# Optimization experiments

Measured on AMD Instinct MI355X. Metric: run time of the kernel, lower is better.

The kernel has to match this reference:

```python
import jax, jax.numpy as jnp
import numpy as np

N_NODES = 8192
N_EDGES = 131072

_DIMS = [
    ("cnn1", 3, 32), ("cnn2", 32, 64), ("cnn3", 64, 128),
    ("gcn1", 128, 256), ("gcn2", 256, 512), ("gcn3", 512, 1024),
    ("cnnd1", 1024, 512), ("cnnd2", 512, 256), ("cnnd3", 256, 128), ("cnnd4", 128, 50),
]


def setup_inputs() -> dict:
    key = jax.random.key(0)
    ks = jax.random.split(key, 2 + 2 * len(_DIMS))
    inp = {
        "x": jax.random.normal(ks[0], (N_NODES, 3), dtype=jnp.float32),
        "edge_index": jax.random.randint(ks[1], (2, N_EDGES), 0, N_NODES, dtype=jnp.int64)
        if jax.config.jax_enable_x64 else
        jax.random.randint(ks[1], (2, N_EDGES), 0, N_NODES, dtype=jnp.int32),
    }
    for i, (name, din, dout) in enumerate(_DIMS):
        scale = 1.0 / np.sqrt(din)
        inp[name + "_w"] = jax.random.normal(ks[2 + 2 * i], (din, dout), dtype=jnp.float32) * scale
        inp[name + "_b"] = jax.random.normal(ks[3 + 2 * i], (dout,), dtype=jnp.float32) * scale
    return inp


def _gcn_norm(edge_index, n, dtype):
    # add self-loops, symmetric normalization D^{-1/2}(A+I)D^{-1/2}
    loop = jnp.arange(n, dtype=edge_index.dtype)
    src = jnp.concatenate([edge_index[0], loop])
    dst = jnp.concatenate([edge_index[1], loop])
    deg = jax.ops.segment_sum(jnp.ones_like(dst, dtype=dtype), dst, num_segments=n)
    dinv = jnp.where(deg > 0, 1.0 / jnp.sqrt(deg), 0.0)
    norm = dinv[src] * dinv[dst]  # [E+N]
    return src, dst, norm


def _forward(x, edge_index,
             cnn1_w, cnn1_b, cnn2_w, cnn2_b, cnn3_w, cnn3_b,
             gcn1_w, gcn1_b, gcn2_w, gcn2_b, gcn3_w, gcn3_b,
             cnnd1_w, cnnd1_b, cnnd2_w, cnnd2_b, cnnd3_w, cnnd3_b, cnnd4_w, cnnd4_b):
    n = x.shape[0]
    src, dst, norm = _gcn_norm(edge_index, n, x.dtype)

    def lin(h, w, b):  # 1x1 Conv1d == per-node linear
        return h @ w + b

    def gcn(h, w, b):
        hl = h @ w                                    # [N, out]
        msg = hl[src] * norm[:, None]                 # gather + scale [E+N, out]
        return jax.ops.segment_sum(msg, dst, num_segments=n) + b

    h = jax.nn.relu(lin(x, cnn1_w, cnn1_b))
    h = jax.nn.relu(lin(h, cnn2_w, cnn2_b))
    h = jax.nn.relu(lin(h, cnn3_w, cnn3_b))
    h = jax.nn.relu(gcn(h, gcn1_w, gcn1_b))
    h = jax.nn.relu(gcn(h, gcn2_w, gcn2_b))
    h = jax.nn.relu(gcn(h, gcn3_w, gcn3_b))
    h = jax.nn.relu(lin(h, cnnd1_w, cnnd1_b))
    h = jax.nn.relu(lin(h, cnnd2_w, cnnd2_b))
    h = jax.nn.relu(lin(h, cnnd3_w, cnnd3_b))
    h = lin(h, cnnd4_w, cnnd4_b)
    return jax.nn.softmax(h, axis=1)  # [N, output_dim]


def reference(x, edge_index,
              cnn1_w, cnn1_b, cnn2_w, cnn2_b, cnn3_w, cnn3_b,
              gcn1_w, gcn1_b, gcn2_w, gcn2_b, gcn3_w, gcn3_b,
              cnnd1_w, cnnd1_b, cnnd2_w, cnnd2_b, cnnd3_w, cnnd3_b, cnnd4_w, cnnd4_b):
    return _forward(x, edge_index,
                    cnn1_w, cnn1_b, cnn2_w, cnn2_b, cnn3_w, cnn3_b,
                    gcn1_w, gcn1_b, gcn2_w, gcn2_b, gcn3_w, gcn3_b,
                    cnnd1_w, cnnd1_b, cnnd2_w, cnnd2_b, cnnd3_w, cnnd3_b, cnnd4_w, cnnd4_b)
```

## Files before the change

kernel.cpp:

```cpp
#include <hip/hip_runtime.h>
#include <math.h>

#define N_NODES 8192
#define N_EDGES 131072

typedef unsigned short u16;
typedef unsigned int u32;
typedef short bf16x8 __attribute__((ext_vector_type(8)));
typedef int v4i __attribute__((ext_vector_type(4)));
typedef float f32x4 __attribute__((ext_vector_type(4)));

__device__ __forceinline__ u16 f2bf(float x) {
    unsigned u = __float_as_uint(x);
    u += 0x7fffu + ((u >> 16) & 1u);
    return (u16)(u >> 16);
}
__device__ __forceinline__ float bf2f(u16 h) { return __uint_as_float(((unsigned)h) << 16); }

#define GLD_LDS(gp, lp) __builtin_amdgcn_global_load_lds( \
    (const __attribute__((address_space(1))) void*)(gp),  \
    (__attribute__((address_space(3))) void*)(lp), 16, 0, 0)

template <int N> __device__ __forceinline__ void wait_vmcnt() {
    if constexpr (N == 0) asm volatile("s_waitcnt vmcnt(0)" ::: "memory");
    else if constexpr (N == 4) asm volatile("s_waitcnt vmcnt(4)" ::: "memory");
    else static_assert(N < 0, "unsupported vmcnt");
}

__device__ __forceinline__ u32 lds_addr(const void* p) {
    return (u32)(size_t)(const __attribute__((address_space(3))) void*)p;
}

__device__ __forceinline__ bf16x8 lds_read_b128(u32 addr) {
    v4i r;
    asm volatile("ds_read_b128 %0, %1" : "=v"(r) : "v"(addr));
    union { v4i i; bf16x8 b; } u;
    u.i = r;
    return u.b;
}

template <int NU> struct UV;
template <> struct UV<1> { typedef u32 T; };
template <> struct UV<2> { typedef uint2 T; };
template <> struct UV<4> { typedef uint4 T; };


__global__ void k_count(const int* __restrict__ ei, int* __restrict__ deg) {
    int e = blockIdx.x * 256 + threadIdx.x;
    if (e < N_EDGES) atomicAdd(&deg[ei[N_EDGES + e]], 1);
}

__global__ __launch_bounds__(1024) void k_scan(const int* __restrict__ deg,
                                               int* __restrict__ rowptr,
                                               int* __restrict__ pos,
                                               float* __restrict__ dinv) {
    __shared__ int sums[1024];
    int t = threadIdx.x;
    int local[8];
    int s = 0;
#pragma unroll
    for (int i = 0; i < 8; ++i) {
        local[i] = deg[t * 8 + i];
        dinv[t * 8 + i] = 1.0f / sqrtf((float)(local[i] + 1));
        s += local[i];
    }
    sums[t] = s;
    __syncthreads();
    for (int off = 1; off < 1024; off <<= 1) {
        int v = (t >= off) ? sums[t - off] : 0;
        __syncthreads();
        sums[t] += v;
        __syncthreads();
    }
    int run = sums[t] - s;
#pragma unroll
    for (int i = 0; i < 8; ++i) {
        rowptr[t * 8 + i] = run;
        pos[t * 8 + i] = run;
        run += local[i];
    }
    if (t == 1023) rowptr[8192] = run;
}

__global__ void k_fill(const int* __restrict__ ei, const float* __restrict__ dinv,
                       int* __restrict__ pos, int* __restrict__ csr_src,
                       float* __restrict__ csr_w) {
    int e = blockIdx.x * 256 + threadIdx.x;
    if (e < N_EDGES) {
        int s = ei[e];
        int t = ei[N_EDGES + e];
        int idx = atomicAdd(&pos[t], 1);
        csr_src[idx] = s;
        csr_w[idx] = dinv[s] * dinv[t];
    }
}

__global__ void k_prep_all(const float* __restrict__ g1w, const float* __restrict__ g2w,
                           const float* __restrict__ g3w, const float* __restrict__ d1w,
                           const float* __restrict__ d2w, const float* __restrict__ d3w,
                           u16* __restrict__ wts, int* __restrict__ deg) {
    int idx = blockIdx.x * 256 + threadIdx.x;
    if (idx < N_NODES) deg[idx] = 0;
    const float* W;
    int local, lgK, N;
    u16 *hi, *lo;
    if (idx < 32768)        { W = g1w; local = idx;           lgK = 7;  N = 256;  hi = wts;           lo = wts + 32768; }
    else if (idx < 163840)  { W = g2w; local = idx - 32768;   lgK = 8;  N = 512;  hi = wts + 65536;   lo = wts + 196608; }
    else if (idx < 688128)  { W = g3w; local = idx - 163840;  lgK = 9;  N = 1024; hi = wts + 327680;  lo = wts + 851968; }
    else if (idx < 1212416) { W = d1w; local = idx - 688128;  lgK = 10; N = 512;  hi = wts + 1376256; lo = wts + 1900544; }
    else if (idx < 1343488) { W = d2w; local = idx - 1212416; lgK = 9;  N = 256;  hi = wts + 2424832; lo = wts + 2555904; }
    else if (idx < 1376256) { W = d3w; local = idx - 1343488; lgK = 8;  N = 128;  hi = wts + 2686976; lo = wts + 2719744; }
    else return;
    int n = local >> lgK;
    int k = local & ((1 << lgK) - 1);
    float v = W[(size_t)k * N + n];
    u16 h = f2bf(v);
    int dst = ((k >> 3) * N + n) * 8 + (k & 7);
    hi[dst] = h;
    lo[dst] = f2bf(v - bf2f(h));
}

__global__ __launch_bounds__(256) void k_enc_fused(const float* __restrict__ x,
                                                   const float* __restrict__ w1, const float* __restrict__ b1,
                                                   const float* __restrict__ w2, const float* __restrict__ b2,
                                                   const float* __restrict__ w3, const float* __restrict__ b3,
                                                   u16* __restrict__ Chi, u16* __restrict__ Clo) {
    __shared__ float lw[10560];
    const int tid = threadIdx.x;
    for (int i = tid; i < 96; i += 256) lw[i] = w1[i];
    for (int i = tid; i < 32; i += 256) lw[96 + i] = b1[i];
    for (int i = tid; i < 2048; i += 256) lw[128 + i] = w2[i];
    for (int i = tid; i < 64; i += 256) lw[2176 + i] = b2[i];
    for (int i = tid; i < 8192; i += 256) lw[2240 + i] = w3[i];
    for (int i = tid; i < 128; i += 256) lw[10432 + i] = b3[i];
    __syncthreads();

    const int lane = tid & 63;
    const int node = blockIdx.x * 4 + (tid >> 6);

    float x0 = x[node * 3 + 0], x1 = x[node * 3 + 1], x2 = x[node * 3 + 2];

    int o1 = lane & 31;
    float h1 = fmaxf(x0 * lw[o1] + x1 * lw[32 + o1] + x2 * lw[64 + o1] + lw[96 + o1], 0.f);

    float h2 = lw[2176 + lane];
#pragma unroll
    for (int k = 0; k < 32; ++k) h2 += __shfl(h1, k) * lw[128 + k * 64 + lane];
    h2 = fmaxf(h2, 0.f);

    float h3a = lw[10432 + lane];
    float h3b = lw[10432 + 64 + lane];
#pragma unroll
    for (int k = 0; k < 64; ++k) {
        float hk = __shfl(h2, k);
        h3a += hk * lw[2240 + k * 128 + lane];
        h3b += hk * lw[2240 + k * 128 + 64 + lane];
    }
    h3a = fmaxf(h3a, 0.f);
    h3b = fmaxf(h3b, 0.f);

    size_t base = (size_t)node * 128;
    u16 ha = f2bf(h3a), hb = f2bf(h3b);
    Chi[base + lane] = ha;
    Chi[base + 64 + lane] = hb;
    Clo[base + lane] = f2bf(h3a - bf2f(ha));
    Clo[base + 64 + lane] = f2bf(h3b - bf2f(hb));
}

__global__ __launch_bounds__(256) void k_d4sm_fused(const float* __restrict__ A,
                                                    const float* __restrict__ W,
                                                    const float* __restrict__ bias,
                                                    float* __restrict__ out) {
    __shared__ float lw[6450];
    const int tid = threadIdx.x;
    for (int i = tid; i < 6400; i += 256) lw[i] = W[i];
    for (int i = tid; i < 50; i += 256) lw[6400 + i] = bias[i];
    __syncthreads();

    const int lane = tid & 63;
    const int node = blockIdx.x * 4 + (tid >> 6);

    float a0 = A[(size_t)node * 128 + lane];
    float a1 = A[(size_t)node * 128 + 64 + lane];

    float acc = (lane < 50) ? lw[6400 + lane] : 0.f;
    int oc = (lane < 50) ? lane : 0;
#pragma unroll
    for (int k = 0; k < 64; ++k) acc += __shfl(a0, k) * lw[k * 50 + oc];
#pragma unroll
    for (int k = 0; k < 64; ++k) acc += __shfl(a1, k) * lw[(64 + k) * 50 + oc];

    float v = (lane < 50) ? acc : -INFINITY;
    float m = v;
#pragma unroll
    for (int off = 32; off; off >>= 1) m = fmaxf(m, __shfl_xor(m, off));
    float e = (lane < 50) ? expf(v - m) : 0.f;
    float s = e;
#pragma unroll
    for (int off = 32; off; off >>= 1) s += __shfl_xor(s, off);
    if (lane < 50) out[(size_t)node * 50 + lane] = e / s;
}

template <int D>
__global__ __launch_bounds__(256) void k_agg_s(const u16* __restrict__ hi_in,
                                               const u16* __restrict__ lo_in,
                                               u16* __restrict__ hi_out,
                                               u16* __restrict__ lo_out,
                                               const int* __restrict__ rowptr,
                                               const int* __restrict__ csr_src,
                                               const float* __restrict__ csr_w,
                                               const float* __restrict__ dinv) {
    constexpr int EPL = D / 64;
    constexpr int NU = EPL / 2;
    using VT = typename UV<NU>::T;
    int node = blockIdx.x * 4 + (threadIdx.x >> 6);
    int lane = threadIdx.x & 63;
    const size_t off = (size_t)node * D + lane * EPL;
    float acc[EPL];
    {
        float dn = dinv[node];
        float w0 = dn * dn;
        u32 hu[NU], lu[NU];
        *(VT*)hu = *(const VT*)(hi_in + off);
        *(VT*)lu = *(const VT*)(lo_in + off);
#pragma unroll
        for (int j = 0; j < NU; ++j) {
            acc[2 * j]     = (__uint_as_float(hu[j] << 16) + __uint_as_float(lu[j] << 16)) * w0;
            acc[2 * j + 1] = (__uint_as_float(hu[j] & 0xffff0000u) + __uint_as_float(lu[j] & 0xffff0000u)) * w0;
        }
    }
#define EDGE_ACC(S, W) do {                                                            \
        size_t so = (size_t)(S) * D + lane * EPL;                                      \
        u32 hu[NU], lu[NU];                                                            \
        *(VT*)hu = *(const VT*)(hi_in + so);                                           \
        *(VT*)lu = *(const VT*)(lo_in + so);                                           \
        _Pragma("unroll")                                                              \
        for (int j = 0; j < NU; ++j) {                                                 \
            acc[2 * j]     += (__uint_as_float(hu[j] << 16) + __uint_as_float(lu[j] << 16)) * (W); \
            acc[2 * j + 1] += (__uint_as_float(hu[j] & 0xffff0000u) + __uint_as_float(lu[j] & 0xffff0000u)) * (W); \
        }                                                                              \
    } while (0)
    int beg = rowptr[node], end = rowptr[node + 1];
    int e = beg;
    for (; e + 2 <= end; e += 2) {
        int s0 = csr_src[e], s1 = csr_src[e + 1];
        float wa = csr_w[e], wb = csr_w[e + 1];
        EDGE_ACC(s0, wa);
        EDGE_ACC(s1, wb);
    }
    if (e < end) EDGE_ACC(csr_src[e], csr_w[e]);
#undef EDGE_ACC
    u32 how[NU], low[NU];
#pragma unroll
    for (int j = 0; j < NU; ++j) {
        u16 h0 = f2bf(acc[2 * j]);     u16 l0 = f2bf(acc[2 * j] - bf2f(h0));
        u16 h1 = f2bf(acc[2 * j + 1]); u16 l1 = f2bf(acc[2 * j + 1] - bf2f(h1));
        how[j] = (u32)h0 | ((u32)h1 << 16);
        low[j] = (u32)l0 | ((u32)l1 << 16);
    }
    *(VT*)(hi_out + off) = *(VT*)how;
    *(VT*)(lo_out + off) = *(VT*)low;
}

template <int D>
__global__ __launch_bounds__(256) void k_agg(const float* __restrict__ h, float* __restrict__ out,
                                             const int* __restrict__ rowptr,
                                             const int* __restrict__ csr_src,
                                             const float* __restrict__ csr_w,
                                             const float* __restrict__ dinv) {
    constexpr int NF2 = D / 128;
    int node = blockIdx.x * 4 + (threadIdx.x >> 6);
    int lane = threadIdx.x & 63;
    const float2* hn = (const float2*)(h + (size_t)node * D);
    float dn = dinv[node];
    float w0 = dn * dn;
    float2 acc[NF2];
#pragma unroll
    for (int j = 0; j < NF2; ++j) {
        float2 v = hn[lane + j * 64];
        acc[j].x = v.x * w0;
        acc[j].y = v.y * w0;
    }
    int beg = rowptr[node], end = rowptr[node + 1];
    for (int e = beg; e < end; ++e) {
        int s = csr_src[e];
        float w = csr_w[e];
        const float2* hs = (const float2*)(h + (size_t)s * D);
#pragma unroll
        for (int j = 0; j < NF2; ++j) {
            float2 v = hs[lane + j * 64];
            acc[j].x += v.x * w;
            acc[j].y += v.y * w;
        }
    }
    float2* op = (float2*)(out + (size_t)node * D);
#pragma unroll
    for (int j = 0; j < NF2; ++j) op[lane + j * 64] = acc[j];
}

template <int OUTS>
__global__ __launch_bounds__(64) void k_linear_small(const float* __restrict__ A,
                                                     const float* __restrict__ W,
                                                     const float* __restrict__ bias,
                                                     float* __restrict__ Cf,
                                                     u16* __restrict__ Chi,
                                                     u16* __restrict__ Clo,
                                                     int K, int N, int relu) {
    int n = blockIdx.y;
    int o = blockIdx.x * 64 + threadIdx.x;
    if (o >= N) return;
    float s = bias[o];
    const float* a = A + (size_t)n * K;
    for (int k = 0; k < K; ++k) s += a[k] * W[(size_t)k * N + o];
    if (relu) s = fmaxf(s, 0.0f);
    if (OUTS == 0) {
        Cf[(size_t)n * N + o] = s;
    } else {
        u16 h = f2bf(s);
        Chi[(size_t)n * N + o] = h;
        Clo[(size_t)n * N + o] = f2bf(s - bf2f(h));
    }
}

template <int OUTS>
__global__ __launch_bounds__(256, 2) void k_gemm_mfma(
    const u16* __restrict__ Ahi, const u16* __restrict__ Alo,
    const u16* __restrict__ Bhi, const u16* __restrict__ Blo,
    const float* __restrict__ bias,
    float* __restrict__ Cf, u16* __restrict__ Chi, u16* __restrict__ Clo,
    int M, int N, int K, int relu) {
    constexpr int BM = 128, BN = 128, WN = 32;
    constexpr int BK = 32;
    constexpr int FM = BM / 16, FN = WN / 16;
    constexpr int ASZ = (BK / 8) * BM * 16;
    constexpr int TOT = 2 * ASZ;
    constexpr int NSTG = TOT / 4096;

    __shared__ char lds0[TOT] __attribute__((aligned(16)));
    __shared__ char lds1[TOT] __attribute__((aligned(16)));

    const int tid = threadIdx.x;
    const int lane = tid & 63;
    const int wave = tid >> 6;

    const int nwg = gridDim.x * gridDim.y;
    const int d = blockIdx.y * gridDim.x + blockIdx.x;
    const int q = nwg >> 3;
    const int lg = (d & 7) * q + (d >> 3);
    const int bx = lg % gridDim.x, by = lg / gridDim.x;
    const int m0 = by * BM, n0 = bx * BN;

    const u16* gp[NSTG];
    int ldo[NSTG];
#pragma unroll
    for (int i = 0; i < NSTG; ++i) {
        int o = i * 4096 + tid * 16;
        ldo[i] = o;
        const u16* base;
        int roff;
        if (o < ASZ) { base = Ahi; roff = o; }
        else         { base = Alo; roff = o - ASZ; }
        int c = roff / (BM * 16);
        int r = (roff % (BM * 16)) / 16;
        gp[i] = base + (size_t)(m0 + r) * K + c * 8;
    }

    const int kc = lane >> 4, rr = lane & 15;
    const int aoff = (kc * BM + rr) * 16;

    const size_t bbase = ((size_t)kc * N + n0 + wave * WN + rr) * 8;
    const size_t bstep = (size_t)4 * N * 8;

    f32x4 acc[FM][FN];
#pragma unroll
    for (int i = 0; i < FM; ++i)
#pragma unroll
        for (int j = 0; j < FN; ++j) acc[i][j] = f32x4{0.f, 0.f, 0.f, 0.f};

    bf16x8 b0h[FN], b0l[FN], b1h[FN], b1l[FN];

#define STAGE(P, KS) do {                                          \
        _Pragma("unroll")                                          \
        for (int i = 0; i < NSTG; ++i)                             \
            GLD_LDS(gp[i] + (KS) * BK, (P) + ldo[i]);              \
    } while (0)

#define LOADB(BH, BL, KS) do {                                                      \
        _Pragma("unroll")                                                           \
        for (int fn = 0; fn < FN; ++fn) {                                           \
            BH[fn] = *(const bf16x8*)(Bhi + bbase + (size_t)(KS) * bstep + fn * 128); \
            BL[fn] = *(const bf16x8*)(Blo + bbase + (size_t)(KS) * bstep + fn * 128); \
        }                                                                           \
    } while (0)

#define STEP(CUR, DST, BHC, BLC, BHD, BLD, KS) do {                                 \
        if ((KS) + 1 < nks) LOADB(BHD, BLD, (KS) + 1);                              \
        __builtin_amdgcn_sched_barrier(0);                                          \
        if ((KS) + 1 < nks) wait_vmcnt<4>(); else wait_vmcnt<0>();                  \
        asm volatile("s_barrier" ::: "memory");                                     \
        if ((KS) + 1 < nks) STAGE(DST, (KS) + 1);                                   \
        const u32 pb_ = lds_addr(CUR);                                              \
        bf16x8 ah[FM], al[FM];                                                      \
        _Pragma("unroll")                                                           \
        for (int fm = 0; fm < FM; ++fm) {                                           \
            ah[fm] = lds_read_b128(pb_ + aoff + fm * 256);                          \
            al[fm] = lds_read_b128(pb_ + ASZ + aoff + fm * 256);                    \
        }                                                                           \
        asm volatile("s_waitcnt lgkmcnt(0)");                                       \
        __builtin_amdgcn_sched_barrier(0);                                          \
        __builtin_amdgcn_s_setprio(1);                                              \
        _Pragma("unroll")                                                           \
        for (int fm = 0; fm < FM; ++fm)                                             \
            _Pragma("unroll")                                                       \
            for (int fn = 0; fn < FN; ++fn) {                                       \
                acc[fm][fn] = __builtin_amdgcn_mfma_f32_16x16x32_bf16(ah[fm], BHC[fn], acc[fm][fn], 0, 0, 0); \
                acc[fm][fn] = __builtin_amdgcn_mfma_f32_16x16x32_bf16(al[fm], BHC[fn], acc[fm][fn], 0, 0, 0); \
                acc[fm][fn] = __builtin_amdgcn_mfma_f32_16x16x32_bf16(ah[fm], BLC[fn], acc[fm][fn], 0, 0, 0); \
            }                                                                       \
        __builtin_amdgcn_s_setprio(0);                                              \
    } while (0)

    const int nks = K / BK;
    LOADB(b0h, b0l, 0);
    STAGE(lds0, 0);
    for (int base = 0; base < nks; base += 2) {
        STEP(lds0, lds1, b0h, b0l, b1h, b1l, base);
        STEP(lds1, lds0, b1h, b1l, b0h, b0l, base + 1);
    }
    asm volatile("" ::: "memory");
#undef STEP
#undef LOADB
#undef STAGE

    const int cr = (lane >> 4) * 4;
    const int cc = lane & 15;
#pragma unroll
    for (int fm = 0; fm < FM; ++fm)
#pragma unroll
        for (int fn = 0; fn < FN; ++fn) {
            int col = n0 + wave * WN + fn * 16 + cc;
            float bv = bias[col];
#pragma unroll
            for (int r = 0; r < 4; ++r) {
                int row = m0 + fm * 16 + cr + r;
                float v = acc[fm][fn][r] + bv;
                if (relu) v = fmaxf(v, 0.f);
                if (OUTS == 0) {
                    Cf[(size_t)row * N + col] = v;
                } else {
                    u16 h = f2bf(v);
                    Chi[(size_t)row * N + col] = h;
                    Clo[(size_t)row * N + col] = f2bf(v - bf2f(h));
                }
            }
        }
}

template <int BM, int BN, int BK, int TM, int TN>
__global__ __launch_bounds__(256) void k_gemm(const float* __restrict__ A,
                                              const float* __restrict__ W,
                                              const float* __restrict__ bias,
                                              float* __restrict__ C,
                                              int M, int N, int K, int relu) {
    constexpr int TX = BN / TN;
    constexpr int TY = BM / TM;
    __shared__ float As[BK][BM + 4];
    __shared__ float Bs[BK][BN];
    int tid = threadIdx.x;
    int tx = tid % TX, ty = tid / TX;
    int m0 = blockIdx.y * BM, n0 = blockIdx.x * BN;
    float acc[TM][TN] = {};
    for (int k0 = 0; k0 < K; k0 += BK) {
        for (int v = tid; v < BM * BK / 4; v += TX * TY) {
            int r = v / (BK / 4);
            int kcp = (v % (BK / 4)) * 4;
            float4 val = *(const float4*)&A[(size_t)(m0 + r) * K + k0 + kcp];
            As[kcp + 0][r] = val.x; As[kcp + 1][r] = val.y;
            As[kcp + 2][r] = val.z; As[kcp + 3][r] = val.w;
        }
        for (int v = tid; v < BK * BN / 4; v += TX * TY) {
            int kr = v / (BN / 4);
            int c = (v % (BN / 4)) * 4;
            *(float4*)&Bs[kr][c] = *(const float4*)&W[(size_t)(k0 + kr) * N + n0 + c];
        }
        __syncthreads();
#pragma unroll
        for (int kk = 0; kk < BK; ++kk) {
            float a[TM], b[TN];
#pragma unroll
            for (int i = 0; i < TM; i += 4) {
                float4 t4 = *(const float4*)&As[kk][ty * TM + i];
                a[i] = t4.x; a[i + 1] = t4.y; a[i + 2] = t4.z; a[i + 3] = t4.w;
            }
#pragma unroll
            for (int j = 0; j < TN; j += 4) {
                float4 t4 = *(const float4*)&Bs[kk][tx * TN + j];
                b[j] = t4.x; b[j + 1] = t4.y; b[j + 2] = t4.z; b[j + 3] = t4.w;
            }
#pragma unroll
            for (int i = 0; i < TM; ++i)
#pragma unroll
                for (int j = 0; j < TN; ++j) acc[i][j] += a[i] * b[j];
        }
        __syncthreads();
    }
#pragma unroll
    for (int i = 0; i < TM; ++i) {
        int row = m0 + ty * TM + i;
#pragma unroll
        for (int j = 0; j < TN; j += 4) {
            int col = n0 + tx * TN + j;
            float4 v;
            v.x = acc[i][j + 0] + bias[col + 0];
            v.y = acc[i][j + 1] + bias[col + 1];
            v.z = acc[i][j + 2] + bias[col + 2];
            v.w = acc[i][j + 3] + bias[col + 3];
            if (relu) {
                v.x = fmaxf(v.x, 0.0f); v.y = fmaxf(v.y, 0.0f);
                v.z = fmaxf(v.z, 0.0f); v.w = fmaxf(v.w, 0.0f);
            }
            *(float4*)&C[(size_t)row * N + col] = v;
        }
    }
}

__global__ __launch_bounds__(256) void k_softmax50(const float* __restrict__ in,
                                                   float* __restrict__ out) {
    int row = blockIdx.x * 4 + (threadIdx.x >> 6);
    int lane = threadIdx.x & 63;
    float v = (lane < 50) ? in[(size_t)row * 50 + lane] : -INFINITY;
    float m = v;
#pragma unroll
    for (int off = 32; off; off >>= 1) m = fmaxf(m, __shfl_xor(m, off));
    float e = (lane < 50) ? expf(v - m) : 0.0f;
    float s = e;
#pragma unroll
    for (int off = 32; off; off >>= 1) s += __shfl_xor(s, off);
    if (lane < 50) out[(size_t)row * 50 + lane] = e / s;
}


extern "C" void kernel_launch(void* const* d_in, const int* in_sizes, int n_in,
                              void* d_out, int out_size, void* d_ws, size_t ws_size,
                              hipStream_t stream) {
    const float* x  = (const float*)d_in[0];
    const int*   ei = (const int*)d_in[1];
    const float *w1  = (const float*)d_in[2],  *b1  = (const float*)d_in[3];
    const float *w2  = (const float*)d_in[4],  *b2  = (const float*)d_in[5];
    const float *w3  = (const float*)d_in[6],  *b3  = (const float*)d_in[7];
    const float *g1w = (const float*)d_in[8],  *g1b = (const float*)d_in[9];
    const float *g2w = (const float*)d_in[10], *g2b = (const float*)d_in[11];
    const float *g3w = (const float*)d_in[12], *g3b = (const float*)d_in[13];
    const float *d1w = (const float*)d_in[14], *d1b = (const float*)d_in[15];
    const float *d2w = (const float*)d_in[16], *d2b = (const float*)d_in[17];
    const float *d3w = (const float*)d_in[18], *d3b = (const float*)d_in[19];
    const float *d4w = (const float*)d_in[20], *d4b = (const float*)d_in[21];
    float* out = (float*)d_out;

    const size_t NEED_NEW = 57016576ull;

    if (ws_size >= NEED_NEW) {
        char* w = (char*)d_ws;
        u16* p0hi = (u16*)w;
        u16* p0lo = (u16*)(w + 16777216);
        u16* p1hi = (u16*)(w + 33554432);
        u16* p1lo = (u16*)(w + 41943040);
        float* f0 = (float*)p1hi;
        u16* wts = (u16*)(w + 50331648);
        u16 *wt1h = wts,            *wt1l = wt1h + 32768;
        u16 *wt2h = wt1l + 32768,   *wt2l = wt2h + 131072;
        u16 *wt3h = wt2l + 131072,  *wt3l = wt3h + 524288;
        u16 *wd1h = wt3l + 524288,  *wd1l = wd1h + 524288;
        u16 *wd2h = wd1l + 524288,  *wd2l = wd2h + 131072;
        u16 *wd3h = wd2l + 131072,  *wd3l = wd3h + 32768;
        char* cs = w + 55836672;
        int*   deg     = (int*)cs;
        int*   rowptr  = deg + N_NODES;
        int*   pos     = rowptr + 8256;
        float* dinv    = (float*)(pos + N_NODES);
        int*   csr_src = (int*)(dinv + N_NODES);
        float* csr_w   = (float*)(csr_src + N_EDGES);

        k_prep_all<<<1376256 / 256, 256, 0, stream>>>(g1w, g2w, g3w, d1w, d2w, d3w, wts, deg);

        k_count<<<N_EDGES / 256, 256, 0, stream>>>(ei, deg);
        k_scan<<<1, 1024, 0, stream>>>(deg, rowptr, pos, dinv);
        k_fill<<<N_EDGES / 256, 256, 0, stream>>>(ei, dinv, pos, csr_src, csr_w);

        k_enc_fused<<<N_NODES / 4, 256, 0, stream>>>(x, w1, b1, w2, b2, w3, b3, p0hi, p0lo);

        k_agg_s<128><<<N_NODES / 4, 256, 0, stream>>>(p0hi, p0lo, p1hi, p1lo, rowptr, csr_src, csr_w, dinv);
        k_gemm_mfma<1><<<dim3(256 / 128, N_NODES / 128), 256, 0, stream>>>(
            p1hi, p1lo, wt1h, wt1l, g1b, nullptr, p0hi, p0lo, N_NODES, 256, 128, 1);
        k_agg_s<256><<<N_NODES / 4, 256, 0, stream>>>(p0hi, p0lo, p1hi, p1lo, rowptr, csr_src, csr_w, dinv);
        k_gemm_mfma<1><<<dim3(512 / 128, N_NODES / 128), 256, 0, stream>>>(
            p1hi, p1lo, wt2h, wt2l, g2b, nullptr, p0hi, p0lo, N_NODES, 512, 256, 1);
        k_agg_s<512><<<N_NODES / 4, 256, 0, stream>>>(p0hi, p0lo, p1hi, p1lo, rowptr, csr_src, csr_w, dinv);
        k_gemm_mfma<1><<<dim3(1024 / 128, N_NODES / 128), 256, 0, stream>>>(
            p1hi, p1lo, wt3h, wt3l, g3b, nullptr, p0hi, p0lo, N_NODES, 1024, 512, 1);
        k_gemm_mfma<1><<<dim3(512 / 128, N_NODES / 128), 256, 0, stream>>>(
            p0hi, p0lo, wd1h, wd1l, d1b, nullptr, p1hi, p1lo, N_NODES, 512, 1024, 1);
        k_gemm_mfma<1><<<dim3(256 / 128, N_NODES / 128), 256, 0, stream>>>(
            p1hi, p1lo, wd2h, wd2l, d2b, nullptr, p0hi, p0lo, N_NODES, 256, 512, 1);
        k_gemm_mfma<0><<<dim3(128 / 128, N_NODES / 128), 256, 0, stream>>>(
            p0hi, p0lo, wd3h, wd3l, d3b, f0, nullptr, nullptr, N_NODES, 128, 256, 1);

        k_d4sm_fused<<<N_NODES / 4, 256, 0, stream>>>(f0, d4w, d4b, out);
    } else {
        float* bufA = (float*)d_ws;
        float* bufB = bufA + (size_t)N_NODES * 1024;
        int*   deg     = (int*)(bufB + (size_t)N_NODES * 512);
        int*   rowptr  = deg + N_NODES;
        int*   pos     = rowptr + 8256;
        float* dinv    = (float*)(pos + N_NODES);
        int*   csr_src = (int*)(dinv + N_NODES);
        float* csr_w   = (float*)(csr_src + N_EDGES);

        hipMemsetAsync(deg, 0, N_NODES * sizeof(int), stream);
        k_count<<<N_EDGES / 256, 256, 0, stream>>>(ei, deg);
        k_scan<<<1, 1024, 0, stream>>>(deg, rowptr, pos, dinv);
        k_fill<<<N_EDGES / 256, 256, 0, stream>>>(ei, dinv, pos, csr_src, csr_w);

        k_linear_small<0><<<dim3(1, N_NODES), 64, 0, stream>>>(x,    w1, b1, bufA, nullptr, nullptr, 3, 32, 1);
        k_linear_small<0><<<dim3(1, N_NODES), 64, 0, stream>>>(bufA, w2, b2, bufB, nullptr, nullptr, 32, 64, 1);
        k_linear_small<0><<<dim3(2, N_NODES), 64, 0, stream>>>(bufB, w3, b3, bufA, nullptr, nullptr, 64, 128, 1);

        k_agg<128><<<N_NODES / 4, 256, 0, stream>>>(bufA, bufB, rowptr, csr_src, csr_w, dinv);
        k_gemm<64, 64, 16, 4, 4><<<dim3(256 / 64, N_NODES / 64), 256, 0, stream>>>(
            bufB, g1w, g1b, bufA, N_NODES, 256, 128, 1);
        k_agg<256><<<N_NODES / 4, 256, 0, stream>>>(bufA, bufB, rowptr, csr_src, csr_w, dinv);
        k_gemm<128, 128, 16, 8, 8><<<dim3(512 / 128, N_NODES / 128), 256, 0, stream>>>(
            bufB, g2w, g2b, bufA, N_NODES, 512, 256, 1);
        k_agg<512><<<N_NODES / 4, 256, 0, stream>>>(bufA, bufB, rowptr, csr_src, csr_w, dinv);
        k_gemm<128, 128, 16, 8, 8><<<dim3(1024 / 128, N_NODES / 128), 256, 0, stream>>>(
            bufB, g3w, g3b, bufA, N_NODES, 1024, 512, 1);
        k_gemm<128, 128, 16, 8, 8><<<dim3(512 / 128, N_NODES / 128), 256, 0, stream>>>(
            bufA, d1w, d1b, bufB, N_NODES, 512, 1024, 1);
        k_gemm<64, 64, 16, 4, 4><<<dim3(256 / 64, N_NODES / 64), 256, 0, stream>>>(
            bufB, d2w, d2b, bufA, N_NODES, 256, 512, 1);
        k_gemm<64, 64, 16, 4, 4><<<dim3(128 / 64, N_NODES / 64), 256, 0, stream>>>(
            bufA, d3w, d3b, bufB, N_NODES, 128, 256, 1);
        k_linear_small<0><<<dim3(1, N_NODES), 64, 0, stream>>>(bufB, d4w, d4b, bufA, nullptr, nullptr, 128, 50, 0);
        k_softmax50<<<N_NODES / 4, 256, 0, stream>>>(bufA, out);
    }
}
```

Before: 280.4 us.

## Replace LDS-staged MFMA GEMM with direct-global-load register GEMM using 2x2 wave tiling

The split-bf16 MFMA GEMM no longer stages A tiles through double-buffered LDS with global_load_lds and barriers. Each wave now loads its own A and B fragments straight from global memory into registers. Waves are arranged 2x2 over a 128x64 tile, so the grid doubles in the N direction. This removes LDS traffic and barrier synchronisation, but A is now reloaded by several waves, which relies on cache hits and loses the explicit prefetch pipelining.

Result: slower. 394.1 us (+40.5%).

```diff
diff --git a/kernel.cpp b/kernel.cpp
--- a/kernel.cpp
+++ b/kernel.cpp
@@ -7,7 +7,6 @@
 typedef unsigned short u16;
 typedef unsigned int u32;
 typedef short bf16x8 __attribute__((ext_vector_type(8)));
-typedef int v4i __attribute__((ext_vector_type(4)));
 typedef float f32x4 __attribute__((ext_vector_type(4)));
 
 __device__ __forceinline__ u16 f2bf(float x) {
@@ -16,28 +15,6 @@
     return (u16)(u >> 16);
 }
 __device__ __forceinline__ float bf2f(u16 h) { return __uint_as_float(((unsigned)h) << 16); }
-
-#define GLD_LDS(gp, lp) __builtin_amdgcn_global_load_lds( \
-    (const __attribute__((address_space(1))) void*)(gp),  \
-    (__attribute__((address_space(3))) void*)(lp), 16, 0, 0)
-
-template <int N> __device__ __forceinline__ void wait_vmcnt() {
-    if constexpr (N == 0) asm volatile("s_waitcnt vmcnt(0)" ::: "memory");
-    else if constexpr (N == 4) asm volatile("s_waitcnt vmcnt(4)" ::: "memory");
-    else static_assert(N < 0, "unsupported vmcnt");
-}
-
-__device__ __forceinline__ u32 lds_addr(const void* p) {
-    return (u32)(size_t)(const __attribute__((address_space(3))) void*)p;
-}
-
-__device__ __forceinline__ bf16x8 lds_read_b128(u32 addr) {
-    v4i r;
-    asm volatile("ds_read_b128 %0, %1" : "=v"(r) : "v"(addr));
-    union { v4i i; bf16x8 b; } u;
-    u.i = r;
-    return u.b;
-}
 
 template <int NU> struct UV;
 template <> struct UV<1> { typedef u32 T; };
@@ -323,25 +300,19 @@
 }
 
 template <int OUTS>
-__global__ __launch_bounds__(256, 2) void k_gemm_mfma(
+__global__ __launch_bounds__(256) void k_gemm_nolds(
     const u16* __restrict__ Ahi, const u16* __restrict__ Alo,
     const u16* __restrict__ Bhi, const u16* __restrict__ Blo,
     const float* __restrict__ bias,
     float* __restrict__ Cf, u16* __restrict__ Chi, u16* __restrict__ Clo,
     int M, int N, int K, int relu) {
-    constexpr int BM = 128, BN = 128, WN = 32;
-    constexpr int BK = 32;
-    constexpr int FM = BM / 16, FN = WN / 16;
-    constexpr int ASZ = (BK / 8) * BM * 16;
-    constexpr int TOT = 2 * ASZ;
-    constexpr int NSTG = TOT / 4096;
-
-    __shared__ char lds0[TOT] __attribute__((aligned(16)));
-    __shared__ char lds1[TOT] __attribute__((aligned(16)));
+    constexpr int BM = 128, BN = 64, WM = 64, WN = 32;
+    constexpr int FM = WM / 16, FN = WN / 16;
 
     const int tid = threadIdx.x;
     const int lane = tid & 63;
     const int wave = tid >> 6;
+    const int wy = wave >> 1, wx = wave & 1;
 
     const int nwg = gridDim.x * gridDim.y;
     const int d = blockIdx.y * gridDim.x + blockIdx.x;
@@ -350,25 +321,17 @@
     const int bx = lg % gridDim.x, by = lg / gridDim.x;
     const int m0 = by * BM, n0 = bx * BN;
 
-    const u16* gp[NSTG];
-    int ldo[NSTG];
-#pragma unroll
-    for (int i = 0; i < NSTG; ++i) {
-        int o = i * 4096 + tid * 16;
-        ldo[i] = o;
-        const u16* base;
-        int roff;
-        if (o < ASZ) { base = Ahi; roff = o; }
-        else         { base = Alo; roff = o - ASZ; }
-        int c = roff / (BM * 16);
-        int r = (roff % (BM * 16)) / 16;
-        gp[i] = base + (size_t)(m0 + r) * K + c * 8;
-    }
-
     const int kc = lane >> 4, rr = lane & 15;
-    const int aoff = (kc * BM + rr) * 16;
-
-    const size_t bbase = ((size_t)kc * N + n0 + wave * WN + rr) * 8;
+
+    const u16* aph[FM];
+    const u16* apl[FM];
+#pragma unroll
+    for (int fm = 0; fm < FM; ++fm) {
+        size_t ro = (size_t)(m0 + wy * 64 + fm * 16 + rr) * K + kc * 8;
+        aph[fm] = Ahi + ro;
+        apl[fm] = Alo + ro;
+    }
+    const size_t bbase = ((size_t)kc * N + n0 + wx * WN + rr) * 8;
     const size_t bstep = (size_t)4 * N * 8;
 
     f32x4 acc[FM][FN];
@@ -377,60 +340,29 @@
 #pragma unroll
         for (int j = 0; j < FN; ++j) acc[i][j] = f32x4{0.f, 0.f, 0.f, 0.f};
 
-    bf16x8 b0h[FN], b0l[FN], b1h[FN], b1l[FN];
-
-#define STAGE(P, KS) do {                                          \
-        _Pragma("unroll")                                          \
-        for (int i = 0; i < NSTG; ++i)                             \
-            GLD_LDS(gp[i] + (KS) * BK, (P) + ldo[i]);              \
-    } while (0)
-
-#define LOADB(BH, BL, KS) do {                                                      \
-        _Pragma("unroll")                                                           \
-        for (int fn = 0; fn < FN; ++fn) {                                           \
-            BH[fn] = *(const bf16x8*)(Bhi + bbase + (size_t)(KS) * bstep + fn * 128); \
-            BL[fn] = *(const bf16x8*)(Blo + bbase + (size_t)(KS) * bstep + fn * 128); \
-        }                                                                           \
-    } while (0)
-
-#define STEP(CUR, DST, BHC, BLC, BHD, BLD, KS) do {                                 \
-        if ((KS) + 1 < nks) LOADB(BHD, BLD, (KS) + 1);                              \
-        __builtin_amdgcn_sched_barrier(0);                                          \
-        if ((KS) + 1 < nks) wait_vmcnt<4>(); else wait_vmcnt<0>();                  \
-        asm volatile("s_barrier" ::: "memory");                                     \
-        if ((KS) + 1 < nks) STAGE(DST, (KS) + 1);                                   \
-        const u32 pb_ = lds_addr(CUR);                                              \
-        bf16x8 ah[FM], al[FM];                                                      \
-        _Pragma("unroll")                                                           \
-        for (int fm = 0; fm < FM; ++fm) {                                           \
-            ah[fm] = lds_read_b128(pb_ + aoff + fm * 256);                          \
-            al[fm] = lds_read_b128(pb_ + ASZ + aoff + fm * 256);                    \
-        }                                                                           \
-        asm volatile("s_waitcnt lgkmcnt(0)");                                       \
-        __builtin_amdgcn_sched_barrier(0);                                          \
-        __builtin_amdgcn_s_setprio(1);                                              \
-        _Pragma("unroll")                                                           \
-        for (int fm = 0; fm < FM; ++fm)                                             \
-            _Pragma("unroll")                                                       \
-            for (int fn = 0; fn < FN; ++fn) {                                       \
-                acc[fm][fn] = __builtin_amdgcn_mfma_f32_16x16x32_bf16(ah[fm], BHC[fn], acc[fm][fn], 0, 0, 0); \
-                acc[fm][fn] = __builtin_amdgcn_mfma_f32_16x16x32_bf16(al[fm], BHC[fn], acc[fm][fn], 0, 0, 0); \
-                acc[fm][fn] = __builtin_amdgcn_mfma_f32_16x16x32_bf16(ah[fm], BLC[fn], acc[fm][fn], 0, 0, 0); \
-            }                                                                       \
-        __builtin_amdgcn_s_setprio(0);                                              \
-    } while (0)
-
-    const int nks = K / BK;
-    LOADB(b0h, b0l, 0);
-    STAGE(lds0, 0);
-    for (int base = 0; base < nks; base += 2) {
-        STEP(lds0, lds1, b0h, b0l, b1h, b1l, base);
-        STEP(lds1, lds0, b1h, b1l, b0h, b0l, base + 1);
-    }
-    asm volatile("" ::: "memory");
-#undef STEP
-#undef LOADB
-#undef STAGE
+    const int nks = K / 32;
+#pragma unroll 4
+    for (int ks = 0; ks < nks; ++ks) {
+        bf16x8 ah[FM], al[FM], bh[FN], bl[FN];
+#pragma unroll
+        for (int fm = 0; fm < FM; ++fm) {
+            ah[fm] = *(const bf16x8*)(aph[fm] + ks * 32);
+            al[fm] = *(const bf16x8*)(apl[fm] + ks * 32);
+        }
+#pragma unroll
+        for (int fn = 0; fn < FN; ++fn) {
+            bh[fn] = *(const bf16x8*)(Bhi + bbase + (size_t)ks * bstep + fn * 128);
+            bl[fn] = *(const bf16x8*)(Blo + bbase + (size_t)ks * bstep + fn * 128);
+        }
+#pragma unroll
+        for (int fm = 0; fm < FM; ++fm)
+#pragma unroll
+            for (int fn = 0; fn < FN; ++fn) {
+                acc[fm][fn] = __builtin_amdgcn_mfma_f32_16x16x32_bf16(ah[fm], bh[fn], acc[fm][fn], 0, 0, 0);
+                acc[fm][fn] = __builtin_amdgcn_mfma_f32_16x16x32_bf16(al[fm], bh[fn], acc[fm][fn], 0, 0, 0);
+                acc[fm][fn] = __builtin_amdgcn_mfma_f32_16x16x32_bf16(ah[fm], bl[fn], acc[fm][fn], 0, 0, 0);
+            }
+    }
 
     const int cr = (lane >> 4) * 4;
     const int cc = lane & 15;
@@ -438,11 +370,11 @@
     for (int fm = 0; fm < FM; ++fm)
 #pragma unroll
         for (int fn = 0; fn < FN; ++fn) {
-            int col = n0 + wave * WN + fn * 16 + cc;
+            int col = n0 + wx * WN + fn * 16 + cc;
             float bv = bias[col];
 #pragma unroll
             for (int r = 0; r < 4; ++r) {
-                int row = m0 + fm * 16 + cr + r;
+                int row = m0 + wy * 64 + fm * 16 + cr + r;
                 float v = acc[fm][fn][r] + bv;
                 if (relu) v = fmaxf(v, 0.f);
                 if (OUTS == 0) {
@@ -590,19 +522,19 @@
         k_enc_fused<<<N_NODES / 4, 256, 0, stream>>>(x, w1, b1, w2, b2, w3, b3, p0hi, p0lo);
 
         k_agg_s<128><<<N_NODES / 4, 256, 0, stream>>>(p0hi, p0lo, p1hi, p1lo, rowptr, csr_src, csr_w, dinv);
-        k_gemm_mfma<1><<<dim3(256 / 128, N_NODES / 128), 256, 0, stream>>>(
+        k_gemm_nolds<1><<<dim3(256 / 64, N_NODES / 128), 256, 0, stream>>>(
             p1hi, p1lo, wt1h, wt1l, g1b, nullptr, p0hi, p0lo, N_NODES, 256, 128, 1);
         k_agg_s<256><<<N_NODES / 4, 256, 0, stream>>>(p0hi, p0lo, p1hi, p1lo, rowptr, csr_src, csr_w, dinv);
-        k_gemm_mfma<1><<<dim3(512 / 128, N_NODES / 128), 256, 0, stream>>>(
+        k_gemm_nolds<1><<<dim3(512 / 64, N_NODES / 128), 256, 0, stream>>>(
             p1hi, p1lo, wt2h, wt2l, g2b, nullptr, p0hi, p0lo, N_NODES, 512, 256, 1);
         k_agg_s<512><<<N_NODES / 4, 256, 0, stream>>>(p0hi, p0lo, p1hi, p1lo, rowptr, csr_src, csr_w, dinv);
-        k_gemm_mfma<1><<<dim3(1024 / 128, N_NODES / 128), 256, 0, stream>>>(
+        k_gemm_nolds<1><<<dim3(1024 / 64, N_NODES / 128), 256, 0, stream>>>(
             p1hi, p1lo, wt3h, wt3l, g3b, nullptr, p0hi, p0lo, N_NODES, 1024, 512, 1);
-        k_gemm_mfma<1><<<dim3(512 / 128, N_NODES / 128), 256, 0, stream>>>(
+        k_gemm_nolds<1><<<dim3(512 / 64, N_NODES / 128), 256, 0, stream>>>(
             p0hi, p0lo, wd1h, wd1l, d1b, nullptr, p1hi, p1lo, N_NODES, 512, 1024, 1);
-        k_gemm_mfma<1><<<dim3(256 / 128, N_NODES / 128), 256, 0, stream>>>(
+        k_gemm_nolds<1><<<dim3(256 / 64, N_NODES / 128), 256, 0, stream>>>(
             p1hi, p1lo, wd2h, wd2l, d2b, nullptr, p0hi, p0lo, N_NODES, 256, 512, 1);
-        k_gemm_mfma<0><<<dim3(128 / 128, N_NODES / 128), 256, 0, stream>>>(
+        k_gemm_nolds<0><<<dim3(128 / 64, N_NODES / 128), 256, 0, stream>>>(
             p0hi, p0lo, wd3h, wd3l, d3b, f0, nullptr, nullptr, N_NODES, 128, 256, 1);
 
         k_d4sm_fused<<<N_NODES / 4, 256, 0, stream>>>(f0, d4w, d4b, out);
```
